# Kernel optimization log

Hardware: AMD Instinct MI355X
Metric: run time of the kernel (lower is better)

Reference implementation:

```python
import jax, jax.numpy as jnp
import numpy as np

EPS = 1e-5

def conv2d(x, w, padding):
    # x: (N, Cin, H, W), w: (Cout, Cin, kh, kw)
    return jax.lax.conv_general_dilated(
        x, w, window_strides=(1, 1),
        padding=[(padding, padding), (padding, padding)],
        dimension_numbers=('NCHW', 'OIHW', 'NCHW'))

def proj_bn_relu(x, w, gamma, beta, mean, var):
    # 1x1 conv + BatchNorm (eval mode, running stats) + ReLU
    y = conv2d(x, w, 0)
    scale = (gamma / jnp.sqrt(var + EPS))[None, :, None, None]
    shift = (beta - mean * gamma / jnp.sqrt(var + EPS))[None, :, None, None]
    return jax.nn.relu(y * scale + shift)

def setup_inputs() -> dict:
    key = jax.random.key(0)
    ks = jax.random.split(key, 16)
    B, Sx, Sy, C1, C2, Co, H, W, K = 2, 4, 4, 64, 64, 64, 128, 128, 3
    inp = {
        'u': jax.random.normal(ks[0], (B, Sx, C1, H, W), jnp.float32),
        'v': jax.random.normal(ks[1], (B, Sy, C2, H, W), jnp.float32),
        'pu_w': jax.random.normal(ks[2], (C1, C1, 1, 1), jnp.float32) * 0.05,
        'pu_gamma': jnp.ones((C1,), jnp.float32),
        'pu_beta': jnp.zeros((C1,), jnp.float32),
        'pu_mean': jax.random.normal(ks[3], (C1,), jnp.float32) * 0.1,
        'pu_var': jax.random.uniform(ks[4], (C1,), jnp.float32, 0.5, 1.5),
        'pv_w': jax.random.normal(ks[5], (C2, C2, 1, 1), jnp.float32) * 0.05,
        'pv_gamma': jnp.ones((C2,), jnp.float32),
        'pv_beta': jnp.zeros((C2,), jnp.float32),
        'pv_mean': jax.random.normal(ks[6], (C2,), jnp.float32) * 0.1,
        'pv_var': jax.random.uniform(ks[7], (C2,), jnp.float32, 0.5, 1.5),
        'conv_w': jax.random.normal(ks[8], (Co, C1 + C2, K, K), jnp.float32) * 0.02,
        'conv_b': jax.random.normal(ks[9], (Co,), jnp.float32) * 0.02,
    }
    return inp

def reference(u, v, pu_w, pu_gamma, pu_beta, pu_mean, pu_var,
              pv_w, pv_gamma, pv_beta, pv_mean, pv_var, conv_w, conv_b):
    B, Sx, C1, H, W = u.shape
    _, Sy, C2, _, _ = v.shape
    pad = 1
    # flatten set dims into batch for the 1x1 proj+BN+ReLU
    uf = proj_bn_relu(u.reshape(B * Sx, C1, H, W), pu_w, pu_gamma, pu_beta, pu_mean, pu_var)
    vf = proj_bn_relu(v.reshape(B * Sy, C2, H, W), pv_w, pv_gamma, pv_beta, pv_mean, pv_var)
    # conv over concat channels is linear -> split weight and broadcast-add,
    # exactly equal to conv(cat(repeat(u), repeat(v))) without materializing
    # the (B,Sx,Sy,C1+C2,H,W) tensor.
    w_u = conv_w[:, :C1]   # (Co, C1, K, K)
    w_v = conv_w[:, C1:]   # (Co, C2, K, K)
    ou = conv2d(uf, w_u, pad)  # (B*Sx, Co, Ho, Wo)
    ov = conv2d(vf, w_v, pad)  # (B*Sy, Co, Ho, Wo)
    Co, Ho, Wo = ou.shape[1], ou.shape[2], ou.shape[3]
    ou = ou.reshape(B, Sx, 1, Co, Ho, Wo)
    ov = ov.reshape(B, 1, Sy, Co, Ho, Wo)
    out = ou + ov + conv_b[None, None, None, :, None, None]
    return out  # (B, Sx, Sy, Co, Ho, Wo)
```

## Files before the change

kernel.cpp:

```cpp
#include <hip/hip_runtime.h>
#include <hip/hip_bf16.h>

#define C   64
#define Hh  128
#define Ww  128
#define HW  16384

typedef __attribute__((ext_vector_type(8))) short bf16x8;
typedef __attribute__((ext_vector_type(4))) float f32x4;

__device__ __forceinline__ unsigned short f2bf(float f) {
    unsigned u = __builtin_bit_cast(unsigned, f);
    unsigned r = (u + 0x7fff + ((u >> 16) & 1)) >> 16;
    return (unsigned short)r;
}

__global__ __launch_bounds__(256, 3) void proj_mfma(
    const float* __restrict__ xu, const float* __restrict__ xv,
    const float* __restrict__ pu_w, const float* __restrict__ pu_g,
    const float* __restrict__ pu_b, const float* __restrict__ pu_m,
    const float* __restrict__ pu_v,
    const float* __restrict__ pv_w, const float* __restrict__ pv_g,
    const float* __restrict__ pv_b, const float* __restrict__ pv_m,
    const float* __restrict__ pv_v,
    const float* __restrict__ conv_w,
    short* __restrict__ wpu, short* __restrict__ wpv,
    short* __restrict__ yu, short* __restrict__ yv)
{
    __shared__ short xs[256 * 72];
    __shared__ short pwl[64 * 72];
    __shared__ float ssh[64];

    const int img16 = blockIdx.y;
    const int sel   = img16 >> 3;
    const int img   = img16 & 7;
    const float* x  = sel ? xv   : xu;
    const float* pw = sel ? pv_w : pu_w;
    const float* pg = sel ? pv_g : pu_g;
    const float* pb = sel ? pv_b : pu_b;
    const float* pm = sel ? pv_m : pu_m;
    const float* pv = sel ? pv_v : pu_v;
    short* y        = sel ? yv   : yu;

    const int pix0 = blockIdx.x * 256;
    const int tid  = threadIdx.x;

    for (int e = tid; e < 2048; e += 256) {
        const int co = e >> 5;
        const int ci0 = (e & 31) * 2;
        const float scale = pg[co] * rsqrtf(pv[co] + 1e-5f);
        const int packed = (int)f2bf(pw[co * 64 + ci0] * scale)
                         | ((int)f2bf(pw[co * 64 + ci0 + 1] * scale) << 16);
        *(int*)&pwl[co * 72 + ci0] = packed;
    }
    if (tid < 64) {
        const float scale = pg[tid] * rsqrtf(pv[tid] + 1e-5f);
        ssh[tid] = pb[tid] - pm[tid] * scale;
    }

    const float* xb = x + (size_t)img * C * HW;
    const int qd = tid & 63;
    const int cp = tid >> 6;
#pragma unroll
    for (int k = 0; k < 8; ++k) {
        const int pairIdx = cp * 8 + k;
        const int ci0 = pairIdx * 2;
        const f32x4 a = *(const f32x4*)&xb[(size_t)ci0 * HW + pix0 + qd * 4];
        const f32x4 b = *(const f32x4*)&xb[(size_t)(ci0 + 1) * HW + pix0 + qd * 4];
#pragma unroll
        for (int j = 0; j < 4; ++j) {
            const int packed = (int)f2bf(a[j]) | ((int)f2bf(b[j]) << 16);
            *(int*)&xs[(qd * 4 + j) * 72 + ci0] = packed;
        }
    }
    __syncthreads();

    const int wq = tid >> 6;
    const int lane = tid & 63;
    const int lx = lane & 15;
    const int q  = lane >> 4;

    f32x4 acc[4][4];
#pragma unroll
    for (int mt = 0; mt < 4; ++mt)
#pragma unroll
        for (int nt = 0; nt < 4; ++nt) acc[mt][nt] = (f32x4){0.f, 0.f, 0.f, 0.f};

#pragma unroll
    for (int kc = 0; kc < 2; ++kc) {
        bf16x8 a[4], b[4];
#pragma unroll
        for (int mt = 0; mt < 4; ++mt)
            a[mt] = *(const bf16x8*)&xs[((wq * 4 + mt) * 16 + lx) * 72 + kc * 32 + q * 8];
#pragma unroll
        for (int nt = 0; nt < 4; ++nt)
            b[nt] = *(const bf16x8*)&pwl[(nt * 16 + lx) * 72 + kc * 32 + q * 8];
#pragma unroll
        for (int mt = 0; mt < 4; ++mt)
#pragma unroll
            for (int nt = 0; nt < 4; ++nt)
                acc[mt][nt] = __builtin_amdgcn_mfma_f32_16x16x32_bf16(a[mt], b[nt], acc[mt][nt], 0, 0, 0);
    }

    __syncthreads();
#pragma unroll
    for (int mt = 0; mt < 4; ++mt)
#pragma unroll
        for (int nt = 0; nt < 4; ++nt)
#pragma unroll
            for (int r = 0; r < 4; ++r) {
                const int px = (wq * 4 + mt) * 16 + q * 4 + r;
                const int co = nt * 16 + lx;
                float vv = acc[mt][nt][r] + ssh[co];
                vv = fmaxf(vv, 0.f);
                xs[px * 72 + co] = (short)f2bf(vv);
            }
    __syncthreads();
    short* yo = y + ((size_t)img * HW + pix0) * C;
#pragma unroll
    for (int it = 0; it < 8; ++it) {
        const int idx = tid + it * 256;
        const int oct = idx & 7, px = idx >> 3;
        *(int4*)&yo[(size_t)px * C + oct * 8] = *(const int4*)&xs[px * 72 + oct * 8];
    }

    if (img16 < 2) {
        short* wpx = img16 ? wpv : wpu;
        const int c = img16;
        for (int idx = blockIdx.x * 256 + tid; idx < 36864; idx += 64 * 256) {
            const int ci = idx & 31;
            const int co = (idx >> 5) & 63;
            const int r3 = idx >> 11;
            const int tap = r3 % 9;
            const int ch  = r3 / 9;
            const float src = conv_w[(size_t)(co * 128 + c * 64 + ch * 32 + ci) * 9 + tap];
            wpx[idx] = (short)f2bf(src);
        }
    }
}

template<bool FUSED>
__global__ __launch_bounds__(256, 4) void conv_fused(
    const short* __restrict__ act, const short* __restrict__ wp,
    const float* __restrict__ oug, const float* __restrict__ bias,
    float* __restrict__ outp)
{
    __shared__ short xs[204 * 68];
    __shared__ float ts[16 * 132];
    __shared__ float sbias[64];

    const int img = blockIdx.y;
    const int tx = blockIdx.x & 3, ty = blockIdx.x >> 2;
    const int h0 = ty * 4, w0 = tx * 32;
    const int tid = threadIdx.x;
    const int wq = tid >> 6;
    const int lane = tid & 63;
    const int lx = lane & 15;
    const int q  = lane >> 4;
    const int q8 = q * 8;

    if (FUSED && tid < 64) sbias[tid] = bias[tid];

    const short* ub = act + (size_t)img * HW * C;
    for (int idx = tid; idx < 1632; idx += 256) {
        const int oct = idx & 7;
        const int cell = idx >> 3;
        const int h = cell / 34, w = cell - h * 34;
        const int gh = h0 - 1 + h, gw = w0 - 1 + w;
        int4 v = {0, 0, 0, 0};
        if (gh >= 0 && gh < Hh && gw >= 0 && gw < Ww)
            v = *(const int4*)&ub[(size_t)(gh * Ww + gw) * C + oct * 8];
        *(int4*)(&xs[cell * 68 + oct * 8]) = v;
    }
    __syncthreads();

    f32x4 acc[4][2];
#pragma unroll
    for (int mt = 0; mt < 4; ++mt)
#pragma unroll
        for (int nt = 0; nt < 2; ++nt) acc[mt][nt] = (f32x4){0.f, 0.f, 0.f, 0.f};

#pragma unroll
    for (int ch = 0; ch < 2; ++ch)
#pragma unroll
        for (int t = 0; t < 9; ++t) {
            const int ky = t / 3;
            const int kx = t - ky * 3;
            bf16x8 a[4], b[2];
#pragma unroll
            for (int mt = 0; mt < 4; ++mt)
                a[mt] = *(const bf16x8*)&wp[(((ch * 9 + t) * 64) + mt * 16 + lx) * 32 + q8];
#pragma unroll
            for (int nt = 0; nt < 2; ++nt) {
                const int cell = (wq + ky) * 34 + nt * 16 + lx + kx;
                b[nt] = *(const bf16x8*)&xs[cell * 68 + ch * 32 + q8];
            }
#pragma unroll
            for (int mt = 0; mt < 4; ++mt)
#pragma unroll
                for (int nt = 0; nt < 2; ++nt)
                    acc[mt][nt] = __builtin_amdgcn_mfma_f32_16x16x32_bf16(a[mt], b[nt], acc[mt][nt], 0, 0, 0);
        }

    if (FUSED) {
#pragma unroll
        for (int mt = 0; mt < 4; ++mt)
#pragma unroll
            for (int nt = 0; nt < 2; ++nt)
#pragma unroll
                for (int r = 0; r < 4; ++r)
                    acc[mt][nt][r] += sbias[mt * 16 + q * 4 + r];
    }

    const int b  = img >> 2;
    const int sy = img & 3;

#pragma unroll
    for (int mt = 0; mt < 4; ++mt) {
        __syncthreads();
#pragma unroll
        for (int nt = 0; nt < 2; ++nt)
#pragma unroll
            for (int r = 0; r < 4; ++r)
                ts[(q * 4 + r) * 132 + wq * 32 + nt * 16 + lx] = acc[mt][nt][r];
        __syncthreads();
        if (!FUSED) {
            float* ob = outp + (size_t)img * C * HW;
#pragma unroll
            for (int k = 0; k < 2; ++k) {
                const int f = tid + k * 256;
                const int co = f >> 5, c2 = f & 31;
                const int px = c2 * 4;
                const int h2 = px >> 5, w2 = px & 31;
                *(f32x4*)&ob[(size_t)(mt * 16 + co) * HW + (h0 + h2) * Ww + w0 + w2] =
                    *(const f32x4*)&ts[co * 132 + c2 * 4];
            }
        } else {
#pragma unroll
            for (int k = 0; k < 2; ++k) {
                const int f = tid + k * 256;
                const int co = f >> 5, c2 = f & 31;
                const int px = c2 * 4;
                const int h2 = px >> 5, w2 = px & 31;
                const size_t off = (size_t)(mt * 16 + co) * HW + (h0 + h2) * Ww + w0 + w2;
                const f32x4 tv = *(const f32x4*)&ts[co * 132 + c2 * 4];
#pragma unroll
                for (int sx = 0; sx < 4; ++sx) {
                    const f32x4 o = *(const f32x4*)&oug[(size_t)(b * 4 + sx) * C * HW + off];
                    f32x4 rr = tv + o;
                    __builtin_nontemporal_store(rr,
                        (f32x4*)&outp[((size_t)((b * 4 + sx) * 4 + sy)) * C * HW + off]);
                }
            }
        }
    }
}

extern "C" void kernel_launch(void* const* d_in, const int* in_sizes, int n_in,
                              void* d_out, int out_size, void* d_ws, size_t ws_size,
                              hipStream_t stream)
{
    const float* u        = (const float*)d_in[0];
    const float* v        = (const float*)d_in[1];
    const float* pu_w     = (const float*)d_in[2];
    const float* pu_gamma = (const float*)d_in[3];
    const float* pu_beta  = (const float*)d_in[4];
    const float* pu_mean  = (const float*)d_in[5];
    const float* pu_var   = (const float*)d_in[6];
    const float* pv_w     = (const float*)d_in[7];
    const float* pv_gamma = (const float*)d_in[8];
    const float* pv_beta  = (const float*)d_in[9];
    const float* pv_mean  = (const float*)d_in[10];
    const float* pv_var   = (const float*)d_in[11];
    const float* conv_w   = (const float*)d_in[12];
    const float* conv_b   = (const float*)d_in[13];
    float* out = (float*)d_out;

    char* ws = (char*)d_ws;
    short* uf  = (short*)(ws);
    short* vf  = (short*)(ws + 16777216);
    float* ou  = (float*)(ws + 33554432);
    char*  aux = ws + 67108864;
    short* wpu = (short*)(aux);
    short* wpv = (short*)(aux + 73728);

    dim3 gp(64, 16);
    proj_mfma<<<gp, 256, 0, stream>>>(u, v,
                                      pu_w, pu_gamma, pu_beta, pu_mean, pu_var,
                                      pv_w, pv_gamma, pv_beta, pv_mean, pv_var,
                                      conv_w, wpu, wpv, uf, vf);

    dim3 gc(128, 8);
    conv_fused<false><<<gc, 256, 0, stream>>>(uf, wpu, nullptr, nullptr, ou);
    conv_fused<true ><<<gc, 256, 0, stream>>>(vf, wpv, ou, conv_b, out);
}
```

Measured before the change: 267.2 us.

## Swizzle proj LDS layout and widen conv per-wave tile to two rows

The projection kernel's activation tile in shared memory moves from a padded stride to an XOR-swizzled 64-short layout. Each thread now packs four channel pairs into one 128-bit LDS store instead of scalar 32-bit stores, which is meant to cut bank conflicts and LDS store count. The conv kernel drops to 128 threads per block, with each wave covering two output rows (4x4 MFMA tiles). This reuses each loaded weight fragment across twice as many pixel tiles and changes the LDS pad to 72, at the cost of more accumulator registers and fewer waves per block.

```diff
diff --git a/kernel.cpp b/kernel.cpp
--- a/kernel.cpp
+++ b/kernel.cpp
@@ -27,7 +27,7 @@
     short* __restrict__ wpu, short* __restrict__ wpv,
     short* __restrict__ yu, short* __restrict__ yv)
 {
-    __shared__ short xs[256 * 72];
+    __shared__ short xs[256 * 64];
     __shared__ short pwl[64 * 72];
     __shared__ float ssh[64];
 
@@ -62,15 +62,27 @@
     const int qd = tid & 63;
     const int cp = tid >> 6;
 #pragma unroll
-    for (int k = 0; k < 8; ++k) {
-        const int pairIdx = cp * 8 + k;
-        const int ci0 = pairIdx * 2;
-        const f32x4 a = *(const f32x4*)&xb[(size_t)ci0 * HW + pix0 + qd * 4];
-        const f32x4 b = *(const f32x4*)&xb[(size_t)(ci0 + 1) * HW + pix0 + qd * 4];
+    for (int kk = 0; kk < 2; ++kk) {
+        int4 pk[4];
+#pragma unroll
+        for (int k4 = 0; k4 < 4; ++k4) {
+            const int ci0 = (cp * 8 + kk * 4 + k4) * 2;
+            const f32x4 a = *(const f32x4*)&xb[(size_t)ci0 * HW + pix0 + qd * 4];
+            const f32x4 b = *(const f32x4*)&xb[(size_t)(ci0 + 1) * HW + pix0 + qd * 4];
+#pragma unroll
+            for (int j = 0; j < 4; ++j) {
+                const int packed = (int)f2bf(a[j]) | ((int)f2bf(b[j]) << 16);
+                if (k4 == 0) pk[j].x = packed;
+                else if (k4 == 1) pk[j].y = packed;
+                else if (k4 == 2) pk[j].z = packed;
+                else pk[j].w = packed;
+            }
+        }
+        const int chunk = cp * 2 + kk;
 #pragma unroll
         for (int j = 0; j < 4; ++j) {
-            const int packed = (int)f2bf(a[j]) | ((int)f2bf(b[j]) << 16);
-            *(int*)&xs[(qd * 4 + j) * 72 + ci0] = packed;
+            const int px = qd * 4 + j;
+            *(int4*)&xs[px * 64 + ((chunk ^ (px & 7)) << 3)] = pk[j];
         }
     }
     __syncthreads();
@@ -90,8 +102,10 @@
     for (int kc = 0; kc < 2; ++kc) {
         bf16x8 a[4], b[4];
 #pragma unroll
-        for (int mt = 0; mt < 4; ++mt)
-            a[mt] = *(const bf16x8*)&xs[((wq * 4 + mt) * 16 + lx) * 72 + kc * 32 + q * 8];
+        for (int mt = 0; mt < 4; ++mt) {
+            const int px = (wq * 4 + mt) * 16 + lx;
+            a[mt] = *(const bf16x8*)&xs[px * 64 + (((kc * 4 + q) ^ (lx & 7)) << 3)];
+        }
 #pragma unroll
         for (int nt = 0; nt < 4; ++nt)
             b[nt] = *(const bf16x8*)&pwl[(nt * 16 + lx) * 72 + kc * 32 + q * 8];
@@ -113,7 +127,7 @@
                 const int co = nt * 16 + lx;
                 float vv = acc[mt][nt][r] + ssh[co];
                 vv = fmaxf(vv, 0.f);
-                xs[px * 72 + co] = (short)f2bf(vv);
+                xs[px * 64 + (co ^ ((px & 7) << 3))] = (short)f2bf(vv);
             }
     __syncthreads();
     short* yo = y + ((size_t)img * HW + pix0) * C;
@@ -121,7 +135,8 @@
     for (int it = 0; it < 8; ++it) {
         const int idx = tid + it * 256;
         const int oct = idx & 7, px = idx >> 3;
-        *(int4*)&yo[(size_t)px * C + oct * 8] = *(const int4*)&xs[px * 72 + oct * 8];
+        *(int4*)&yo[(size_t)px * C + oct * 8] =
+            *(const int4*)&xs[px * 64 + ((oct ^ (px & 7)) << 3)];
     }
 
     if (img16 < 2) {
@@ -140,12 +155,12 @@
 }
 
 template<bool FUSED>
-__global__ __launch_bounds__(256, 4) void conv_fused(
+__global__ __launch_bounds__(128, 2) void conv_fused(
     const short* __restrict__ act, const short* __restrict__ wp,
     const float* __restrict__ oug, const float* __restrict__ bias,
     float* __restrict__ outp)
 {
-    __shared__ short xs[204 * 68];
+    __shared__ short xs[204 * 72];
     __shared__ float ts[16 * 132];
     __shared__ float sbias[64];
 
@@ -162,7 +177,7 @@
     if (FUSED && tid < 64) sbias[tid] = bias[tid];
 
     const short* ub = act + (size_t)img * HW * C;
-    for (int idx = tid; idx < 1632; idx += 256) {
+    for (int idx = tid; idx < 1632; idx += 128) {
         const int oct = idx & 7;
         const int cell = idx >> 3;
         const int h = cell / 34, w = cell - h * 34;
@@ -170,15 +185,15 @@
         int4 v = {0, 0, 0, 0};
         if (gh >= 0 && gh < Hh && gw >= 0 && gw < Ww)
             v = *(const int4*)&ub[(size_t)(gh * Ww + gw) * C + oct * 8];
-        *(int4*)(&xs[cell * 68 + oct * 8]) = v;
+        *(int4*)(&xs[cell * 72 + oct * 8]) = v;
     }
     __syncthreads();
 
-    f32x4 acc[4][2];
+    f32x4 acc[4][4];
 #pragma unroll
     for (int mt = 0; mt < 4; ++mt)
 #pragma unroll
-        for (int nt = 0; nt < 2; ++nt) acc[mt][nt] = (f32x4){0.f, 0.f, 0.f, 0.f};
+        for (int nt = 0; nt < 4; ++nt) acc[mt][nt] = (f32x4){0.f, 0.f, 0.f, 0.f};
 
 #pragma unroll
     for (int ch = 0; ch < 2; ++ch)
@@ -186,19 +201,19 @@
         for (int t = 0; t < 9; ++t) {
             const int ky = t / 3;
             const int kx = t - ky * 3;
-            bf16x8 a[4], b[2];
+            bf16x8 a[4], b[4];
 #pragma unroll
             for (int mt = 0; mt < 4; ++mt)
                 a[mt] = *(const bf16x8*)&wp[(((ch * 9 + t) * 64) + mt * 16 + lx) * 32 + q8];
 #pragma unroll
-            for (int nt = 0; nt < 2; ++nt) {
-                const int cell = (wq + ky) * 34 + nt * 16 + lx + kx;
-                b[nt] = *(const bf16x8*)&xs[cell * 68 + ch * 32 + q8];
+            for (int nt = 0; nt < 4; ++nt) {
+                const int cell = (2 * wq + (nt >> 1) + ky) * 34 + (nt & 1) * 16 + lx + kx;
+                b[nt] = *(const bf16x8*)&xs[cell * 72 + ch * 32 + q8];
             }
 #pragma unroll
             for (int mt = 0; mt < 4; ++mt)
 #pragma unroll
-                for (int nt = 0; nt < 2; ++nt)
+                for (int nt = 0; nt < 4; ++nt)
                     acc[mt][nt] = __builtin_amdgcn_mfma_f32_16x16x32_bf16(a[mt], b[nt], acc[mt][nt], 0, 0, 0);
         }
 
@@ -206,7 +221,7 @@
 #pragma unroll
         for (int mt = 0; mt < 4; ++mt)
 #pragma unroll
-            for (int nt = 0; nt < 2; ++nt)
+            for (int nt = 0; nt < 4; ++nt)
 #pragma unroll
                 for (int r = 0; r < 4; ++r)
                     acc[mt][nt][r] += sbias[mt * 16 + q * 4 + r];
@@ -219,16 +234,17 @@
     for (int mt = 0; mt < 4; ++mt) {
         __syncthreads();
 #pragma unroll
-        for (int nt = 0; nt < 2; ++nt)
+        for (int nt = 0; nt < 4; ++nt)
 #pragma unroll
             for (int r = 0; r < 4; ++r)
-                ts[(q * 4 + r) * 132 + wq * 32 + nt * 16 + lx] = acc[mt][nt][r];
+                ts[(q * 4 + r) * 132 + (2 * wq + (nt >> 1)) * 32 + (nt & 1) * 16 + lx]
+                    = acc[mt][nt][r];
         __syncthreads();
         if (!FUSED) {
             float* ob = outp + (size_t)img * C * HW;
 #pragma unroll
-            for (int k = 0; k < 2; ++k) {
-                const int f = tid + k * 256;
+            for (int k = 0; k < 4; ++k) {
+                const int f = tid + k * 128;
                 const int co = f >> 5, c2 = f & 31;
                 const int px = c2 * 4;
                 const int h2 = px >> 5, w2 = px & 31;
@@ -237,8 +253,8 @@
             }
         } else {
 #pragma unroll
-            for (int k = 0; k < 2; ++k) {
-                const int f = tid + k * 256;
+            for (int k = 0; k < 4; ++k) {
+                const int f = tid + k * 128;
                 const int co = f >> 5, c2 = f & 31;
                 const int px = c2 * 4;
                 const int h2 = px >> 5, w2 = px & 31;
@@ -291,6 +307,6 @@
                                       conv_w, wpu, wpv, uf, vf);
 
     dim3 gc(128, 8);
-    conv_fused<false><<<gc, 256, 0, stream>>>(uf, wpu, nullptr, nullptr, ou);
-    conv_fused<true ><<<gc, 256, 0, stream>>>(vf, wpv, ou, conv_b, out);
+    conv_fused<false><<<gc, 128, 0, stream>>>(uf, wpu, nullptr, nullptr, ou);
+    conv_fused<true ><<<gc, 128, 0, stream>>>(vf, wpv, ou, conv_b, out);
 }
```

Result: faster. 258.9 us (-3.1%).
